# Kernel tuning notes

Measured on AMD Instinct MI355X. Metric: run time of the kernel, lower is better.

## Reference

```python
import jax, jax.numpy as jnp
import numpy as np


def setup_inputs() -> dict:
    key = jax.random.key(0)
    x = jax.random.normal(key, (16, 512, 512, 8), dtype=jnp.float32)
    # 3x3 structuring element with center False: neighbors-only local max
    mask = jnp.array([[True, True, True],
                      [True, False, True],
                      [True, True, True]])
    return {"x": x, "mask": mask}


def reference(x, mask):
    # Equivalent of tf.nn.dilation2d(x, where(mask, 0, -inf), SAME, stride 1):
    # masked_max[b,i,j,c] = max over (di,dj) in mask of x[b,i+di-ph, j+dj-pw, c]
    # (out-of-bounds treated as -inf, matching dilation's identity padding).
    kh, kw = mask.shape  # small static window (e.g. 3x3)
    H, W = x.shape[1], x.shape[2]
    ph, pw = (kh - 1) // 2, (kw - 1) // 2
    neg_inf = jnp.asarray(-jnp.inf, x.dtype)
    xp = jnp.pad(x, ((0, 0), (ph, kh - 1 - ph), (pw, kw - 1 - pw), (0, 0)),
                 constant_values=-np.inf)
    masked_max = jnp.full_like(x, -np.inf)
    for di in range(kh):          # fixed small kernel loop (9 taps), not a data-dim loop
        for dj in range(kw):
            win = xp[:, di:di + H, dj:dj + W, :]
            masked_max = jnp.maximum(masked_max, jnp.where(mask[di, dj], win, neg_inf))
    # suppressed = cast(x > masked_max) * x
    return (x > masked_max).astype(x.dtype) * x
```

## Files before the change

kernel.cpp:

```cpp
#include <hip/hip_runtime.h>
#include <math.h>

constexpr int Hdim = 512;
constexpr int Wdim = 512;

__global__ __launch_bounds__(256) void nms_kernel(
    const float4* __restrict__ x,
    const unsigned char* __restrict__ mask_bytes,
    float4* __restrict__ out,
    int total4)
{
    const int* mask_ints = (const int*)mask_bytes;
    bool int_layout = true;
    #pragma unroll
    for (int i = 0; i < 9; ++i) {
        int v = mask_ints[i];
        int_layout = int_layout && (v == 0 || v == 1);
    }
    unsigned mbits = 0;
    #pragma unroll
    for (int i = 0; i < 9; ++i) {
        bool b = int_layout ? (mask_ints[i] != 0) : (mask_bytes[i] != 0);
        mbits |= (unsigned)b << i;
    }

    int idx = blockIdx.x * blockDim.x + threadIdx.x;
    if (idx >= total4) return;

    int w = (idx >> 1) & (Wdim - 1);
    int h = (idx >> 10) & (Hdim - 1);

    float4 c = x[idx];
    float mx = -INFINITY, my = -INFINITY, mz = -INFINITY, mw = -INFINITY;

    #pragma unroll
    for (int di = 0; di < 3; ++di) {
        int hh = h + di - 1;
        bool hok = (hh >= 0) && (hh < Hdim);
        #pragma unroll
        for (int dj = 0; dj < 3; ++dj) {
            if (!((mbits >> (di * 3 + dj)) & 1u)) continue;
            int ww = w + dj - 1;
            bool ok = hok && (ww >= 0) && (ww < Wdim);
            if (ok) {
                float4 v = x[idx + ((di - 1) * Wdim + (dj - 1)) * 2];
                mx = fmaxf(mx, v.x);
                my = fmaxf(my, v.y);
                mz = fmaxf(mz, v.z);
                mw = fmaxf(mw, v.w);
            }
        }
    }

    float4 o;
    o.x = (c.x > mx) ? c.x : 0.0f;
    o.y = (c.y > my) ? c.y : 0.0f;
    o.z = (c.z > mz) ? c.z : 0.0f;
    o.w = (c.w > mw) ? c.w : 0.0f;
    out[idx] = o;
}

extern "C" void kernel_launch(void* const* d_in, const int* in_sizes, int n_in,
                              void* d_out, int out_size, void* d_ws, size_t ws_size,
                              hipStream_t stream) {
    const float4* x = (const float4*)d_in[0];
    const unsigned char* mask = (const unsigned char*)d_in[1];
    float4* out = (float4*)d_out;

    int total4 = out_size / 4;
    int block = 256;
    int grid = (total4 + block - 1) / block;
    nms_kernel<<<grid, block, 0, stream>>>(x, mask, out, total4);
}
```

Baseline: 255.4 us.

## Process eight rows per thread with sliding register window of neighbor rows

Each thread now computes eight vertically consecutive outputs, keeping three rows of left/center/right float4 values in registers and loading only one new row per step. This cuts redundant global/cache loads from nine per output to about three. It trades parallelism (8x fewer threads) and more registers for less memory traffic.

```diff
diff --git a/kernel.cpp b/kernel.cpp
--- a/kernel.cpp
+++ b/kernel.cpp
@@ -1,63 +1,88 @@
 #include <hip/hip_runtime.h>
 #include <math.h>
 
+
 constexpr int Hdim = 512;
 constexpr int Wdim = 512;
+constexpr int HPT  = 8;
+constexpr int ROW  = Wdim * 2;
+
+__device__ __forceinline__ float4 f4max(float4 a, float4 b) {
+    return make_float4(fmaxf(a.x,b.x), fmaxf(a.y,b.y), fmaxf(a.z,b.z), fmaxf(a.w,b.w));
+}
 
 __global__ __launch_bounds__(256) void nms_kernel(
     const float4* __restrict__ x,
     const unsigned char* __restrict__ mask_bytes,
-    float4* __restrict__ out,
-    int total4)
+    float4* __restrict__ out)
 {
-    const int* mask_ints = (const int*)mask_bytes;
-    bool int_layout = true;
+    const int* mi = (const int*)mask_bytes;
+    bool intlay = true;
     #pragma unroll
-    for (int i = 0; i < 9; ++i) {
-        int v = mask_ints[i];
-        int_layout = int_layout && (v == 0 || v == 1);
-    }
-    unsigned mbits = 0;
+    for (int i = 0; i < 9; ++i) { int v = mi[i]; intlay = intlay && (v == 0 || v == 1); }
+    bool m[9];
     #pragma unroll
-    for (int i = 0; i < 9; ++i) {
-        bool b = int_layout ? (mask_ints[i] != 0) : (mask_bytes[i] != 0);
-        mbits |= (unsigned)b << i;
-    }
+    for (int i = 0; i < 9; ++i) m[i] = intlay ? (mi[i] != 0) : (mask_bytes[i] != 0);
 
-    int idx = blockIdx.x * blockDim.x + threadIdx.x;
-    if (idx >= total4) return;
+    int gid = blockIdx.x * blockDim.x + threadIdx.x;
+    int c4 = gid & 1;
+    int w  = (gid >> 1) & (Wdim - 1);
+    int hg = (gid >> 10) & 63;
+    int n  = gid >> 16;
+    int h0 = hg * HPT;
 
-    int w = (idx >> 1) & (Wdim - 1);
-    int h = (idx >> 10) & (Hdim - 1);
+    const float4 NEG = make_float4(-INFINITY, -INFINITY, -INFINITY, -INFINITY);
+    bool aok = (w > 0), cok = (w < Wdim - 1);
+    int ao = aok ? -2 : 0;
+    int co = cok ?  2 : 0;
 
-    float4 c = x[idx];
-    float mx = -INFINITY, my = -INFINITY, mz = -INFINITY, mw = -INFINITY;
+    long base = ((long)((n * Hdim + h0) * Wdim + w)) * 2 + c4;
+
+    auto loadrow = [&](long rb, float4& a, float4& b, float4& c) {
+        float4 at = x[rb + ao];
+        b         = x[rb];
+        float4 ct = x[rb + co];
+        a = aok ? at : NEG;
+        c = cok ? ct : NEG;
+    };
+
+    auto vmax = [&](float4 r0, float4 r1, float4 r2, bool b0, bool b1, bool b2) {
+        float4 v = NEG;
+        if (b0) v = f4max(v, r0);
+        if (b1) v = f4max(v, r1);
+        if (b2) v = f4max(v, r2);
+        return v;
+    };
+
+    float4 a0, b0, c0, a1, b1, c1;
+    if (h0 > 0) loadrow(base - ROW, a0, b0, c0);
+    else        { a0 = NEG; b0 = NEG; c0 = NEG; }
+    loadrow(base, a1, b1, c1);
 
     #pragma unroll
-    for (int di = 0; di < 3; ++di) {
-        int hh = h + di - 1;
-        bool hok = (hh >= 0) && (hh < Hdim);
-        #pragma unroll
-        for (int dj = 0; dj < 3; ++dj) {
-            if (!((mbits >> (di * 3 + dj)) & 1u)) continue;
-            int ww = w + dj - 1;
-            bool ok = hok && (ww >= 0) && (ww < Wdim);
-            if (ok) {
-                float4 v = x[idx + ((di - 1) * Wdim + (dj - 1)) * 2];
-                mx = fmaxf(mx, v.x);
-                my = fmaxf(my, v.y);
-                mz = fmaxf(mz, v.z);
-                mw = fmaxf(mw, v.w);
-            }
-        }
+    for (int s = 0; s < HPT; ++s) {
+        int h = h0 + s;
+        float4 a2, b2, c2;
+        if (h + 1 < Hdim) loadrow(base + (long)(s + 1) * ROW, a2, b2, c2);
+        else              { a2 = NEG; b2 = NEG; c2 = NEG; }
+
+        float4 va = vmax(a0, a1, a2, m[0], m[3], m[6]);
+        float4 vb = vmax(b0, b1, b2, m[1], m[4], m[7]);
+        float4 vc = vmax(c0, c1, c2, m[2], m[5], m[8]);
+        float4 mm = f4max(f4max(va, vb), vc);
+
+        float4 ctr = b1;
+        float4 o;
+        o.x = (ctr.x > mm.x) ? ctr.x : 0.0f;
+        o.y = (ctr.y > mm.y) ? ctr.y : 0.0f;
+        o.z = (ctr.z > mm.z) ? ctr.z : 0.0f;
+        o.w = (ctr.w > mm.w) ? ctr.w : 0.0f;
+        out[base + (long)s * ROW] = o;
+
+        a0 = a1; a1 = a2;
+        b0 = b1; b1 = b2;
+        c0 = c1; c1 = c2;
     }
-
-    float4 o;
-    o.x = (c.x > mx) ? c.x : 0.0f;
-    o.y = (c.y > my) ? c.y : 0.0f;
-    o.z = (c.z > mz) ? c.z : 0.0f;
-    o.w = (c.w > mw) ? c.w : 0.0f;
-    out[idx] = o;
 }
 
 extern "C" void kernel_launch(void* const* d_in, const int* in_sizes, int n_in,
@@ -67,8 +92,8 @@
     const unsigned char* mask = (const unsigned char*)d_in[1];
     float4* out = (float4*)d_out;
 
-    int total4 = out_size / 4;
+    int total = 16 * (Hdim / HPT) * Wdim * 2;
     int block = 256;
-    int grid = (total4 + block - 1) / block;
-    nms_kernel<<<grid, block, 0, stream>>>(x, mask, out, total4);
+    int grid = total / block;
+    nms_kernel<<<grid, block, 0, stream>>>(x, mask, out);
 }
```

Measured after the change: 238.2 us. 6.7% less time.
